# Kernel optimization log

Measured on AMD Instinct MI355X. Metric: run time of the kernel, lower is better.

Reference implementation:

```python
import jax, jax.numpy as jnp
import numpy as np

BN_EPS = 1e-5


def setup_inputs() -> dict:
    key = jax.random.key(0)
    k1, k2 = jax.random.split(key)
    B, IN, OUT = 16384, 2048, 2048
    x = jax.random.normal(k1, (B, IN), dtype=jnp.float32)
    weight = jax.random.normal(k2, (OUT, IN), dtype=jnp.float32) * 0.05
    gamma = jnp.ones((OUT,), dtype=jnp.float32)
    beta = jnp.zeros((OUT,), dtype=jnp.float32)
    return {"x": x, "weight": weight, "gamma": gamma, "beta": beta}


def reference(x, weight, gamma, beta):
    # Deterministic binarization: sign(w) in {-1, +1} (0 maps to +1)
    w_bin = jnp.where(weight >= 0, 1.0, -1.0).astype(weight.dtype)
    # Linear (no bias): y = x @ W_bin^T  -> [B, OUT]
    y = jnp.einsum("bi,oi->bo", x, w_bin)
    # BatchNorm1d, training mode: biased batch statistics over batch dim
    mean = jnp.mean(y, axis=0)
    var = jnp.mean(jnp.square(y - mean), axis=0)
    y = (y - mean) * (gamma * jax.lax.rsqrt(var + BN_EPS)) + beta
    # ReLU activation
    return jax.nn.relu(y)
```

## Files before the change

kernel.cpp:

```cpp
#include <hip/hip_runtime.h>
#include <stdint.h>

#define B_DIM   16384
#define IN_DIM  2048
#define OUT_DIM 2048
#define BN_EPS  1e-5f

typedef int    i32x4 __attribute__((ext_vector_type(4)));
typedef unsigned short u16x4 __attribute__((ext_vector_type(4)));


__device__ __forceinline__ unsigned short f2bf_rne(float f) {
    unsigned u = __builtin_bit_cast(unsigned, f);
    return (unsigned short)((u + 0x7fffu + ((u >> 16) & 1u)) >> 16);
}
__device__ __forceinline__ float bf2f(unsigned short h) {
    unsigned u = ((unsigned)h) << 16;
    return __builtin_bit_cast(float, u);
}

__device__ __forceinline__ void gl_lds16(const void* g, void* l) {
    __builtin_amdgcn_global_load_lds(
        (const __attribute__((address_space(1))) unsigned int*)g,
        (__attribute__((address_space(3))) unsigned int*)l,
        16, 0, 0);
}

__device__ __forceinline__ int pack4(float a, float b, float c, float d, float inv) {
    int q0 = (int)rintf(a * inv) & 255;
    int q1 = (int)rintf(b * inv) & 255;
    int q2 = (int)rintf(c * inv) & 255;
    int q3 = (int)rintf(d * inv) & 255;
    return q0 | (q1 << 8) | (q2 << 16) | (q3 << 24);
}

__global__ __launch_bounds__(256) void quantize_x_kernel(
        const float4* __restrict__ x4, int* __restrict__ xq,
        float* __restrict__ scales) {
    __shared__ float wmax[4];
    const int row = blockIdx.x;
    const int t = threadIdx.x;
    const float4* xr = x4 + (size_t)row * 512;
    float4 a = xr[t];
    float4 b = xr[t + 256];
    float m = fmaxf(fmaxf(fabsf(a.x), fabsf(a.y)), fmaxf(fabsf(a.z), fabsf(a.w)));
    m = fmaxf(m, fmaxf(fmaxf(fabsf(b.x), fabsf(b.y)), fmaxf(fabsf(b.z), fabsf(b.w))));
#pragma unroll
    for (int off = 32; off >= 1; off >>= 1) m = fmaxf(m, __shfl_xor(m, off));
    if ((t & 63) == 0) wmax[t >> 6] = m;
    __syncthreads();
    m = fmaxf(fmaxf(wmax[0], wmax[1]), fmaxf(wmax[2], wmax[3]));
    m = fmaxf(m, 1e-20f);
    const float inv = 127.0f / m;
    if (t == 0) scales[row] = m * (1.0f / 127.0f);
    int* xo = xq + (size_t)row * 512;
    xo[t]       = pack4(a.x, a.y, a.z, a.w, inv);
    xo[t + 256] = pack4(b.x, b.y, b.z, b.w, inv);
}

__global__ __launch_bounds__(256) void convert_w_kernel(
        const float4* __restrict__ w, int* __restrict__ wq,
        float4* __restrict__ stats ) {
    int id = blockIdx.x * 256 + threadIdx.x;
    if (id < 1024) stats[id] = make_float4(0.f, 0.f, 0.f, 0.f);
    float4 a = w[id];
    int b0 = (a.x < 0.f) ? 0xFF : 0x01;
    int b1 = (a.y < 0.f) ? 0xFF : 0x01;
    int b2 = (a.z < 0.f) ? 0xFF : 0x01;
    int b3 = (a.w < 0.f) ? 0xFF : 0x01;
    wq[id] = b0 | (b1 << 8) | (b2 << 16) | (b3 << 24);
}

__global__ __launch_bounds__(256, 2) void gemm_bn_kernel(
        const char* __restrict__ A, const char* __restrict__ Bw,
        const float* __restrict__ scales,
        unsigned short* __restrict__ Yb,
        float* __restrict__ colsum, float* __restrict__ colsumsq) {
    __shared__ char sA[2 * 128 * 64];
    __shared__ char sB[2 * 128 * 64];

    const int tid  = threadIdx.x;
    const int wave = tid >> 6;
    const int lane = tid & 63;
    const int wm = wave >> 1;
    const int wn = wave & 1;
    const int lr = lane & 15;
    const int lq = lane >> 4;

    const int b  = blockIdx.x;
    const int lb = (b & 7) * 256 + (b >> 3);
    const int bm = (lb >> 4) * 128;
    const int bn = (lb & 15) * 128;

    const int srow = lane >> 2;
    const int scol = (lane & 3) * 16;
    const char* gp[8];
    char* lp[8];
#pragma unroll
    for (int q = 0; q < 8; ++q) {
        int g    = wave * 8 + q;
        int isB  = g >> 4;
        int slab = (g >> 3) & 1;
        int c    = g & 7;
        const char* basep = isB ? Bw : A;
        int tileoff       = isB ? bn : bm;
        gp[q] = basep + (size_t)(tileoff + c * 16 + srow) * IN_DIM
                      + slab * 64 + scol;
        char* sbase = isB ? sB : sA;
        lp[q] = sbase + slab * 8192 + c * 1024 + lane * 16;
    }

    const int aoff = (wm * 64 + lr) * 64 + lq * 16;
    const int boff = (wn * 64 + lr) * 64 + lq * 16;

    i32x4 acc[4][4];
#pragma unroll
    for (int i = 0; i < 4; ++i)
#pragma unroll
        for (int j = 0; j < 4; ++j) {
            i32x4 z = {0, 0, 0, 0};
            acc[i][j] = z;
        }

    for (int k0 = 0; k0 < IN_DIM; k0 += 128) {
        __syncthreads();
#pragma unroll
        for (int q = 0; q < 8; ++q)
            gl_lds16(gp[q] + k0, lp[q]);
        __syncthreads();

#pragma unroll
        for (int kh = 0; kh < 2; ++kh) {
            const char* aB = sA + kh * 8192 + aoff;
            const char* bB = sB + kh * 8192 + boff;
            i32x4 av[4], bv[4];
#pragma unroll
            for (int i = 0; i < 4; ++i)
                av[i] = *(const i32x4*)(aB + i * 1024);
#pragma unroll
            for (int j = 0; j < 4; ++j)
                bv[j] = *(const i32x4*)(bB + j * 1024);
#pragma unroll
            for (int i = 0; i < 4; ++i)
#pragma unroll
                for (int j = 0; j < 4; ++j)
                    acc[i][j] = __builtin_amdgcn_mfma_i32_16x16x64_i8(
                        av[i], bv[j], acc[i][j], 0, 0, 0);
        }
    }

    float colS[4], colQ[4];
#pragma unroll
    for (int j = 0; j < 4; ++j) { colS[j] = 0.f; colQ[j] = 0.f; }

#pragma unroll
    for (int i = 0; i < 4; ++i) {
        const int row0 = bm + wm * 64 + i * 16 + lq * 4;
        float sc[4];
#pragma unroll
        for (int r = 0; r < 4; ++r) sc[r] = scales[row0 + r];
#pragma unroll
        for (int r = 0; r < 4; ++r) {
            size_t base = (size_t)(row0 + r) * OUT_DIM + bn + wn * 64 + lr;
#pragma unroll
            for (int j = 0; j < 4; ++j) {
                float v = (float)acc[i][j][r] * sc[r];
                Yb[base + j * 16] = f2bf_rne(v);
                colS[j] += v;
                colQ[j] += v * v;
            }
        }
    }

#pragma unroll
    for (int j = 0; j < 4; ++j) {
        float s = colS[j], q = colQ[j];
        s += __shfl_xor(s, 16); s += __shfl_xor(s, 32);
        q += __shfl_xor(q, 16); q += __shfl_xor(q, 32);
        if (lq == 0) {
            int col = bn + wn * 64 + j * 16 + lr;
            atomicAdd(&colsum[col], s);
            atomicAdd(&colsumsq[col], q);
        }
    }
}

__global__ __launch_bounds__(256) void finalize_kernel(
        const float* __restrict__ colsum, const float* __restrict__ colsumsq,
        const float* __restrict__ gamma, const float* __restrict__ beta,
        float* __restrict__ scale, float* __restrict__ bias) {
    int n = blockIdx.x * 256 + threadIdx.x;
    if (n < OUT_DIM) {
        const float inv = 1.f / (float)B_DIM;
        float mean = colsum[n] * inv;
        float var  = colsumsq[n] * inv - mean * mean;
        float sc   = gamma[n] * rsqrtf(var + BN_EPS);
        scale[n] = sc;
        bias[n]  = beta[n] - mean * sc;
    }
}

__global__ __launch_bounds__(256) void bn_relu_bf16_kernel(
        const u16x4* __restrict__ yb, float4* __restrict__ out,
        const float4* __restrict__ scale4, const float4* __restrict__ bias4) {
    int base = blockIdx.x * 512 + threadIdx.x;
#pragma unroll
    for (int p = 0; p < 2; ++p) {
        int id = base + p * 256;
        int c4 = id & (OUT_DIM / 4 - 1);
        u16x4 h = yb[id];
        float4 s = scale4[c4];
        float4 bb = bias4[c4];
        float4 v;
        v.x = fmaxf(fmaf(bf2f(h[0]), s.x, bb.x), 0.f);
        v.y = fmaxf(fmaf(bf2f(h[1]), s.y, bb.y), 0.f);
        v.z = fmaxf(fmaf(bf2f(h[2]), s.z, bb.z), 0.f);
        v.w = fmaxf(fmaf(bf2f(h[3]), s.w, bb.w), 0.f);
        out[id] = v;
    }
}

extern "C" void kernel_launch(void* const* d_in, const int* in_sizes, int n_in,
                              void* d_out, int out_size, void* d_ws, size_t ws_size,
                              hipStream_t stream) {
    const float* x     = (const float*)d_in[0];
    const float* w     = (const float*)d_in[1];
    const float* gamma = (const float*)d_in[2];
    const float* beta  = (const float*)d_in[3];
    float* out = (float*)d_out;

    char* ws = (char*)d_ws;
    const size_t XQ_OFF = 0;
    const size_t WQ_OFF = XQ_OFF + (size_t)B_DIM * IN_DIM;
    const size_t YB_OFF = WQ_OFF + (size_t)OUT_DIM * IN_DIM;
    const size_t ST_OFF = YB_OFF + (size_t)B_DIM * OUT_DIM * 2;
    const size_t SC_OFF = ST_OFF + 8192 * 4;

    char* xq = ws + XQ_OFF;
    char* wq = ws + WQ_OFF;
    unsigned short* yb = (unsigned short*)(ws + YB_OFF);
    float* colsum   = (float*)(ws + ST_OFF);
    float* colsumsq = colsum + 2048;
    float* scale    = colsum + 4096;
    float* bias     = colsum + 6144;
    float* scales   = (float*)(ws + SC_OFF);

    quantize_x_kernel<<<B_DIM, 256, 0, stream>>>(
        (const float4*)x, (int*)xq, scales);
    convert_w_kernel<<<4096, 256, 0, stream>>>(
        (const float4*)w, (int*)wq, (float4*)colsum);
    gemm_bn_kernel<<<2048, 256, 0, stream>>>(
        xq, wq, scales, yb, colsum, colsumsq);
    finalize_kernel<<<8, 256, 0, stream>>>(
        colsum, colsumsq, gamma, beta, scale, bias);
    bn_relu_bf16_kernel<<<16384, 256, 0, stream>>>(
        (const u16x4*)yb, (float4*)out, (const float4*)scale,
        (const float4*)bias);
}
```

Before: 330.5 us.

## Rebuild int8 GEMM with 256x256 tiles and double-buffered swizzled LDS pipeline

The GEMM+stats kernel moves from 128x128 tiles with 256 threads to 256x256 tiles with 512 threads. It now uses a 128KB double-buffered LDS ring, XOR-swizzled so LDS reads avoid bank conflicts. Global-to-LDS loads for the next K step are issued between the MFMA phases, with explicit vmcnt waits, barriers and s_setprio, so memory traffic overlaps compute. The larger tile halves global reuse traffic per output, but it raises register pressure to 128 accumulators per thread, limits occupancy to one block per CU because of LDS size, and adds many barriers.

After: 328.7 us. About the same (-0.5%).

```diff
diff --git a/kernel.cpp b/kernel.cpp
--- a/kernel.cpp
+++ b/kernel.cpp
@@ -71,91 +71,145 @@
     wq[id] = b0 | (b1 << 8) | (b2 << 16) | (b3 << 24);
 }
 
-__global__ __launch_bounds__(256, 2) void gemm_bn_kernel(
+__global__ __launch_bounds__(512, 2) void gemm_bn_kernel(
         const char* __restrict__ A, const char* __restrict__ Bw,
         const float* __restrict__ scales,
         unsigned short* __restrict__ Yb,
         float* __restrict__ colsum, float* __restrict__ colsumsq) {
-    __shared__ char sA[2 * 128 * 64];
-    __shared__ char sB[2 * 128 * 64];
+    __shared__ __align__(16) char smem[131072];
 
     const int tid  = threadIdx.x;
     const int wave = tid >> 6;
     const int lane = tid & 63;
-    const int wm = wave >> 1;
-    const int wn = wave & 1;
+    const int wm = wave >> 2;
+    const int wn = wave & 3;
     const int lr = lane & 15;
     const int lq = lane >> 4;
 
     const int b  = blockIdx.x;
-    const int lb = (b & 7) * 256 + (b >> 3);
-    const int bm = (lb >> 4) * 128;
-    const int bn = (lb & 15) * 128;
-
-    const int srow = lane >> 2;
-    const int scol = (lane & 3) * 16;
-    const char* gp[8];
-    char* lp[8];
-#pragma unroll
-    for (int q = 0; q < 8; ++q) {
-        int g    = wave * 8 + q;
-        int isB  = g >> 4;
-        int slab = (g >> 3) & 1;
-        int c    = g & 7;
-        const char* basep = isB ? Bw : A;
-        int tileoff       = isB ? bn : bm;
-        gp[q] = basep + (size_t)(tileoff + c * 16 + srow) * IN_DIM
-                      + slab * 64 + scol;
-        char* sbase = isB ? sB : sA;
-        lp[q] = sbase + slab * 8192 + c * 1024 + lane * 16;
-    }
-
-    const int aoff = (wm * 64 + lr) * 64 + lq * 16;
-    const int boff = (wn * 64 + lr) * 64 + lq * 16;
-
-    i32x4 acc[4][4];
-#pragma unroll
-    for (int i = 0; i < 4; ++i)
+    const int lb = (b & 7) * 64 + (b >> 3);
+    const int bm = (lb >> 3) * 256;
+    const int bn = (lb & 7) * 256;
+
+    const int swz16 = (((tid & 7) ^ ((tid >> 3) & 7)) << 4);
+    const char* gA = A  + (size_t)(bm + (tid >> 3)) * IN_DIM + swz16;
+    const char* gB = Bw + (size_t)(bn + (tid >> 3)) * IN_DIM + swz16;
+    const int ldst = tid << 4;
+
+    const int aRd = wm * 16384 + lr * 128;
+    const int bRd = wn * 8192  + lr * 128;
+    const int sl0 = ((lq    ) ^ (lr & 7)) << 4;
+    const int sl1 = ((lq + 4) ^ (lr & 7)) << 4;
+
+    i32x4 acc[8][4];
+#pragma unroll
+    for (int i = 0; i < 8; ++i)
 #pragma unroll
         for (int j = 0; j < 4; ++j) {
             i32x4 z = {0, 0, 0, 0};
             acc[i][j] = z;
         }
 
-    for (int k0 = 0; k0 < IN_DIM; k0 += 128) {
-        __syncthreads();
-#pragma unroll
-        for (int q = 0; q < 8; ++q)
-            gl_lds16(gp[q] + k0, lp[q]);
-        __syncthreads();
-
-#pragma unroll
-        for (int kh = 0; kh < 2; ++kh) {
-            const char* aB = sA + kh * 8192 + aoff;
-            const char* bB = sB + kh * 8192 + boff;
-            i32x4 av[4], bv[4];
-#pragma unroll
-            for (int i = 0; i < 4; ++i)
-                av[i] = *(const i32x4*)(aB + i * 1024);
-#pragma unroll
-            for (int j = 0; j < 4; ++j)
-                bv[j] = *(const i32x4*)(bB + j * 1024);
-#pragma unroll
-            for (int i = 0; i < 4; ++i)
-#pragma unroll
-                for (int j = 0; j < 4; ++j)
-                    acc[i][j] = __builtin_amdgcn_mfma_i32_16x16x64_i8(
-                        av[i], bv[j], acc[i][j], 0, 0, 0);
-        }
-    }
+#define VM_WAIT(N) asm volatile("s_waitcnt vmcnt(" #N ")" ::: "memory")
+#define LGKM0()    asm volatile("s_waitcnt lgkmcnt(0)" ::: "memory")
+#define BAR()      __builtin_amdgcn_s_barrier()
+
+#define MM16(IB) \
+    _Pragma("unroll") for (int i = 0; i < 4; ++i) \
+    _Pragma("unroll") for (int j = 0; j < 4; ++j) \
+        acc[(IB) + i][j] = __builtin_amdgcn_mfma_i32_16x16x64_i8( \
+            av[i], bv[j], acc[(IB) + i][j], 0, 0, 0)
+
+    {
+        char* An = smem;
+        char* Bn = smem + 32768;
+        gl_lds16(gB + 0 * 131072, Bn + 0 * 8192 + ldst);
+        gl_lds16(gB + 1 * 131072, Bn + 1 * 8192 + ldst);
+        gl_lds16(gB + 2 * 131072, Bn + 2 * 8192 + ldst);
+        gl_lds16(gB + 3 * 131072, Bn + 3 * 8192 + ldst);
+        gl_lds16(gA + 0 * 131072, An + 0 * 8192 + ldst);
+        gl_lds16(gA + 2 * 131072, An + 2 * 8192 + ldst);
+        gl_lds16(gA + 1 * 131072, An + 1 * 8192 + ldst);
+        gl_lds16(gA + 3 * 131072, An + 3 * 8192 + ldst);
+        VM_WAIT(2);
+        BAR();
+    }
+
+#define GTILE(t_, LAST_) do {                                                  \
+    const char* Ab = smem + (((t_) & 1) ? 65536 : 0);                          \
+    const char* Bb = Ab + 32768;                                               \
+    char* An = smem + (((t_) & 1) ? 0 : 65536);                                \
+    char* Bn = An + 32768;                                                     \
+    const size_t kn = (size_t)((t_) + 1) * 128;                                \
+    i32x4 av[4], bv[4];                                                        \
+                        \
+    _Pragma("unroll") for (int j = 0; j < 4; ++j)                              \
+        bv[j] = *(const i32x4*)(Bb + bRd + j * 2048 + sl0);                    \
+    _Pragma("unroll") for (int i = 0; i < 4; ++i)                              \
+        av[i] = *(const i32x4*)(Ab + aRd + i * 2048 + sl0);                    \
+    if (!(LAST_)) {                                                            \
+        gl_lds16(gB + kn          , Bn + 0 * 8192 + ldst);                     \
+        gl_lds16(gB + kn + 131072 , Bn + 1 * 8192 + ldst);                     \
+        gl_lds16(gB + kn + 262144 , Bn + 2 * 8192 + ldst);                     \
+        gl_lds16(gB + kn + 393216 , Bn + 3 * 8192 + ldst);                     \
+    }                                                                          \
+    if (LAST_) { VM_WAIT(0); } else { VM_WAIT(4); }       \
+    BAR(); LGKM0();                                                            \
+    __builtin_amdgcn_s_setprio(1);                                             \
+    MM16(0);                                                                   \
+    __builtin_amdgcn_s_setprio(0);                                             \
+    BAR();                                                                     \
+                   \
+    _Pragma("unroll") for (int i = 0; i < 4; ++i)                              \
+        av[i] = *(const i32x4*)(Ab + aRd + (i + 4) * 2048 + sl0);              \
+    if (!(LAST_)) {                                                            \
+        gl_lds16(gA + kn          , An + 0 * 8192 + ldst);                     \
+        gl_lds16(gA + kn + 262144 , An + 2 * 8192 + ldst);                     \
+        gl_lds16(gA + kn + 131072 , An + 1 * 8192 + ldst);                     \
+        gl_lds16(gA + kn + 393216 , An + 3 * 8192 + ldst);                     \
+    }                                                                          \
+    BAR(); LGKM0();                                                            \
+    __builtin_amdgcn_s_setprio(1);                                             \
+    MM16(4);                                                                   \
+    __builtin_amdgcn_s_setprio(0);                                             \
+    BAR();                                                                     \
+                               \
+    _Pragma("unroll") for (int j = 0; j < 4; ++j)                              \
+        bv[j] = *(const i32x4*)(Bb + bRd + j * 2048 + sl1);                    \
+    _Pragma("unroll") for (int i = 0; i < 4; ++i)                              \
+        av[i] = *(const i32x4*)(Ab + aRd + i * 2048 + sl1);                    \
+    BAR(); LGKM0();                                                            \
+    __builtin_amdgcn_s_setprio(1);                                             \
+    MM16(0);                                                                   \
+    __builtin_amdgcn_s_setprio(0);                                             \
+    BAR();                                                                     \
+      \
+    _Pragma("unroll") for (int i = 0; i < 4; ++i)                              \
+        av[i] = *(const i32x4*)(Ab + aRd + (i + 4) * 2048 + sl1);              \
+    VM_WAIT(2);                                                                \
+    BAR(); LGKM0();                                                            \
+    __builtin_amdgcn_s_setprio(1);                                             \
+    MM16(4);                                                                   \
+    __builtin_amdgcn_s_setprio(0);                                             \
+    BAR();                                                                     \
+} while (0)
+
+    for (int t = 0; t < 15; ++t) GTILE(t, 0);
+    GTILE(15, 1);
+
+#undef GTILE
+#undef MM16
+#undef VM_WAIT
+#undef LGKM0
+#undef BAR
 
     float colS[4], colQ[4];
 #pragma unroll
     for (int j = 0; j < 4; ++j) { colS[j] = 0.f; colQ[j] = 0.f; }
 
 #pragma unroll
-    for (int i = 0; i < 4; ++i) {
-        const int row0 = bm + wm * 64 + i * 16 + lq * 4;
+    for (int i = 0; i < 8; ++i) {
+        const int row0 = bm + wm * 128 + i * 16 + lq * 4;
         float sc[4];
 #pragma unroll
         for (int r = 0; r < 4; ++r) sc[r] = scales[row0 + r];
@@ -249,7 +303,7 @@
         (const float4*)x, (int*)xq, scales);
     convert_w_kernel<<<4096, 256, 0, stream>>>(
         (const float4*)w, (int*)wq, (float4*)colsum);
-    gemm_bn_kernel<<<2048, 256, 0, stream>>>(
+    gemm_bn_kernel<<<512, 512, 0, stream>>>(
         xq, wq, scales, yb, colsum, colsumsq);
     finalize_kernel<<<8, 256, 0, stream>>>(
         colsum, colsumsq, gamma, beta, scale, bias);
```

## Double-buffer int8 GEMM with swizzled LDS and larger 256x128 block tiles

Applied to the files above, without the earlier changes.

The int8 MFMA GEMM now runs 512-thread blocks that each compute a 256x128 output tile, so every B tile is reused across twice as many rows. The K loop steps by 64 with two LDS buffers: the global-to-LDS loads for step t+2 are issued while step t+1 is still landing, using explicit vmcnt waits and barriers instead of a full sync around every load. The 16-byte chunk addresses in LDS are XOR-swizzled to cut bank conflicts on the fragment reads, and s_setprio raises wave priority around the MFMA burst. In exchange the kernel uses more LDS and registers per block, which may limit occupancy, and the fully unrolled 32-step loop grows code size.

Result: no change. 335.4 us (+1.5%).

```diff
diff --git a/kernel.cpp b/kernel.cpp
--- a/kernel.cpp
+++ b/kernel.cpp
@@ -71,13 +71,12 @@
     wq[id] = b0 | (b1 << 8) | (b2 << 16) | (b3 << 24);
 }
 
-__global__ __launch_bounds__(256, 2) void gemm_bn_kernel(
+__global__ __launch_bounds__(512, 4) void gemm_bn_kernel(
         const char* __restrict__ A, const char* __restrict__ Bw,
         const float* __restrict__ scales,
         unsigned short* __restrict__ Yb,
         float* __restrict__ colsum, float* __restrict__ colsumsq) {
-    __shared__ char sA[2 * 128 * 64];
-    __shared__ char sB[2 * 128 * 64];
+    __shared__ __align__(16) char smem[2 * 24576];
 
     const int tid  = threadIdx.x;
     const int wave = tid >> 6;
@@ -88,30 +87,19 @@
     const int lq = lane >> 4;
 
     const int b  = blockIdx.x;
-    const int lb = (b & 7) * 256 + (b >> 3);
-    const int bm = (lb >> 4) * 128;
+    const int lb = (b & 7) * 128 + (b >> 3);
+    const int bm = (lb >> 4) * 256;
     const int bn = (lb & 15) * 128;
 
-    const int srow = lane >> 2;
-    const int scol = (lane & 3) * 16;
-    const char* gp[8];
-    char* lp[8];
-#pragma unroll
-    for (int q = 0; q < 8; ++q) {
-        int g    = wave * 8 + q;
-        int isB  = g >> 4;
-        int slab = (g >> 3) & 1;
-        int c    = g & 7;
-        const char* basep = isB ? Bw : A;
-        int tileoff       = isB ? bn : bm;
-        gp[q] = basep + (size_t)(tileoff + c * 16 + srow) * IN_DIM
-                      + slab * 64 + scol;
-        char* sbase = isB ? sB : sA;
-        lp[q] = sbase + slab * 8192 + c * 1024 + lane * 16;
-    }
-
-    const int aoff = (wm * 64 + lr) * 64 + lq * 16;
-    const int boff = (wn * 64 + lr) * 64 + lq * 16;
+    const int swz16 = (((tid & 3) ^ ((tid >> 3) & 3)) << 4);
+    const char* gA0 = A  + (size_t)(bm + (tid >> 2)) * IN_DIM + swz16;
+    const char* gA1 = gA0 + (size_t)128 * IN_DIM;
+    const char* gB0 = Bw + (size_t)(bn + (tid >> 2)) * IN_DIM + swz16;
+    const int ldst = tid << 4;
+
+    const int ps   = ((lq ^ ((lr >> 1) & 3)) << 4);
+    const int aoff = (wm * 64 + lr) * 64 + ps;
+    const int boff = 16384 + (wn * 64 + lr) * 64 + ps;
 
     i32x4 acc[4][4];
 #pragma unroll
@@ -122,32 +110,56 @@
             acc[i][j] = z;
         }
 
-    for (int k0 = 0; k0 < IN_DIM; k0 += 128) {
-        __syncthreads();
-#pragma unroll
-        for (int q = 0; q < 8; ++q)
-            gl_lds16(gp[q] + k0, lp[q]);
-        __syncthreads();
-
-#pragma unroll
-        for (int kh = 0; kh < 2; ++kh) {
-            const char* aB = sA + kh * 8192 + aoff;
-            const char* bB = sB + kh * 8192 + boff;
-            i32x4 av[4], bv[4];
-#pragma unroll
-            for (int i = 0; i < 4; ++i)
-                av[i] = *(const i32x4*)(aB + i * 1024);
+#define VM_WAIT(N) asm volatile("s_waitcnt vmcnt(" #N ")" ::: "memory")
+#define BAR()      __builtin_amdgcn_s_barrier()
+#define STAGE(buf_, k_) do {                                   \
+    char* d = smem + (buf_) * 24576;                           \
+    gl_lds16(gA0 + (k_), d + ldst);                            \
+    gl_lds16(gA1 + (k_), d + 8192 + ldst);                     \
+    gl_lds16(gB0 + (k_), d + 16384 + ldst);                    \
+} while (0)
+
+    STAGE(0, 0);
+    STAGE(1, 64);
+    VM_WAIT(3);
+    BAR();
+
+    const int NT = IN_DIM / 64;
+#pragma unroll
+    for (int t = 0; t < NT; ++t) {
+        const int cur = t & 1;
+        const char* Sb = smem + cur * 24576;
+        i32x4 av[4], bv[4];
+#pragma unroll
+        for (int i = 0; i < 4; ++i)
+            av[i] = *(const i32x4*)(Sb + aoff + i * 1024);
+#pragma unroll
+        for (int j = 0; j < 4; ++j)
+            bv[j] = *(const i32x4*)(Sb + boff + j * 1024);
+
+        __builtin_amdgcn_s_setprio(1);
+#pragma unroll
+        for (int i = 0; i < 4; ++i)
 #pragma unroll
             for (int j = 0; j < 4; ++j)
-                bv[j] = *(const i32x4*)(bB + j * 1024);
-#pragma unroll
-            for (int i = 0; i < 4; ++i)
-#pragma unroll
-                for (int j = 0; j < 4; ++j)
-                    acc[i][j] = __builtin_amdgcn_mfma_i32_16x16x64_i8(
-                        av[i], bv[j], acc[i][j], 0, 0, 0);
-        }
-    }
+                acc[i][j] = __builtin_amdgcn_mfma_i32_16x16x64_i8(
+                    av[i], bv[j], acc[i][j], 0, 0, 0);
+        __builtin_amdgcn_s_setprio(0);
+
+        if (t + 2 < NT) {
+            BAR();
+            STAGE(cur, (size_t)(t + 2) * 64);
+            VM_WAIT(3);
+            BAR();
+        } else if (t + 1 < NT) {
+            VM_WAIT(0);
+            BAR();
+        }
+    }
+
+#undef STAGE
+#undef VM_WAIT
+#undef BAR
 
     float colS[4], colQ[4];
 #pragma unroll
@@ -249,7 +261,7 @@
         (const float4*)x, (int*)xq, scales);
     convert_w_kernel<<<4096, 256, 0, stream>>>(
         (const float4*)w, (int*)wq, (float4*)colsum);
-    gemm_bn_kernel<<<2048, 256, 0, stream>>>(
+    gemm_bn_kernel<<<1024, 512, 0, stream>>>(
         xq, wq, scales, yb, colsum, colsumsq);
     finalize_kernel<<<8, 256, 0, stream>>>(
         colsum, colsumsq, gamma, beta, scale, bias);
```
